# Optimization experiments

Measured on AMD Instinct MI355X. Metric: run time of the kernel, lower is better.

The kernel has to match this reference:

```python
import jax, jax.numpy as jnp
import numpy as np

B, N, D, H = 4, 2048, 512, 8
HD = D // H  # 64


def setup_inputs() -> dict:
    key = jax.random.key(0)
    ks = jax.random.split(key, 12)
    s = 0.02
    return {
        "x": jax.random.normal(ks[0], (B, N, D), jnp.float32),
        "freqs": jax.random.normal(ks[1], (B, N, HD // 2), jnp.float32),
        # weights stored as (in, out); torch Linear applies x @ W.T + b
        "wqkv_w": jax.random.normal(ks[2], (D, 3 * D), jnp.float32) * s,
        "wqkv_b": jax.random.normal(ks[3], (3 * D,), jnp.float32) * s,
        "out_w": jax.random.normal(ks[4], (D, D), jnp.float32) * s,
        "out_b": jax.random.normal(ks[5], (D,), jnp.float32) * s,
        "ffn1_w": jax.random.normal(ks[6], (2 * D, 2 * D), jnp.float32) * s,
        "ffn1_b": jax.random.normal(ks[7], (2 * D,), jnp.float32) * s,
        "ln_g": jnp.ones((2 * D,), jnp.float32),
        "ln_b": jnp.zeros((2 * D,), jnp.float32),
        "ffn2_w": jax.random.normal(ks[8], (2 * D, D), jnp.float32) * s,
        "ffn2_b": jax.random.normal(ks[9], (D,), jnp.float32) * s,
    }


def _rope(t, cos, sin):
    # t: [B,H,N,HD]; cos/sin: [B,1,N,HD/2]
    x1, x2 = t[..., ::2], t[..., 1::2]
    return jnp.stack([x1 * cos - x2 * sin, x1 * sin + x2 * cos], axis=-1).reshape(t.shape)


def reference(x, freqs, wqkv_w, wqkv_b, out_w, out_b,
              ffn1_w, ffn1_b, ln_g, ln_b, ffn2_w, ffn2_b):
    b, n, d = x.shape
    h, hd = H, d // H
    qkv = x @ wqkv_w + wqkv_b                      # [B,N,3D]
    q, k, v = jnp.split(qkv, 3, axis=-1)
    to_heads = lambda t: t.reshape(b, n, h, hd).transpose(0, 2, 1, 3)  # [B,H,N,HD]
    q, k, v = to_heads(q), to_heads(k), to_heads(v)
    cos = jnp.cos(freqs)[:, None]                  # [B,1,N,HD/2]
    sin = jnp.sin(freqs)[:, None]
    q = _rope(q, cos, sin)
    k = _rope(k, cos, sin)
    scale = hd ** -0.5
    attn = jax.nn.softmax(jnp.einsum('bhqd,bhkd->bhqk', q, k) * scale, axis=-1)
    msg = jnp.einsum('bhqk,bhkd->bhqd', attn, v).transpose(0, 2, 1, 3).reshape(b, n, d)
    msg = msg @ out_w + out_b
    # FFN on concat([x, msg]): Linear -> LayerNorm -> GELU(exact) -> Linear
    hcat = jnp.concatenate([x, msg], axis=-1) @ ffn1_w + ffn1_b   # [B,N,2D]
    mu = hcat.mean(-1, keepdims=True)
    var = hcat.var(-1, keepdims=True)
    hcat = (hcat - mu) * jax.lax.rsqrt(var + 1e-5) * ln_g + ln_b
    hcat = jax.nn.gelu(hcat, approximate=False)
    return x + hcat @ ffn2_w + ffn2_b
```

## Files before the change

### kernel.cpp

```cpp
#include <hip/hip_runtime.h>
#include <hip/hip_bf16.h>
#include <math.h>

typedef __bf16 bf16;
typedef __bf16 bf16x2 __attribute__((ext_vector_type(2)));
typedef __bf16 bf16x4 __attribute__((ext_vector_type(4)));
typedef __bf16 bf16x8 __attribute__((ext_vector_type(8)));
typedef float f32x4 __attribute__((ext_vector_type(4)));
typedef float f32x16 __attribute__((ext_vector_type(16)));

#define MFMA16(a, b, c) __builtin_amdgcn_mfma_f32_16x16x32_bf16(a, b, c, 0, 0, 0)
#define MFMA32(a, b, c) __builtin_amdgcn_mfma_f32_32x32x16_bf16(a, b, c, 0, 0, 0)


__global__ __launch_bounds__(256) void prep_kernel(
    const float* __restrict__ wqkv_w, const float* __restrict__ out_w,
    const float* __restrict__ ffn1_w, const float* __restrict__ ffn2_w,
    const float* __restrict__ x, const float* __restrict__ freqs,
    const float* __restrict__ ffn1_b, const float* __restrict__ out_b,
    bf16* __restrict__ wqkv_t, bf16* __restrict__ ffn2_t,
    bf16* __restrict__ fused_t, bf16* __restrict__ ffn1bt,
    bf16* __restrict__ out_cast, bf16* __restrict__ cat,
    float* __restrict__ bias_f, unsigned* __restrict__ tab)
{
    const int bid = blockIdx.x, tid = threadIdx.x;
    __shared__ bf16 tile[32][33];
    __shared__ float red[256];
    if (bid >= 6672) {
        int i = (bid - 6672) * 1024 + tid * 4;
        const float4 f = *(const float4*)(&freqs[i]);
        float s0, c0, s1, c1, s2, c2, s3, c3;
        __sincosf(f.x, &s0, &c0); __sincosf(f.y, &s1, &c1);
        __sincosf(f.z, &s2, &c2); __sincosf(f.w, &s3, &c3);
        union { bf16x2 h2; unsigned u; } p0, p1, p2, p3;
        p0.h2[0] = (bf16)c0; p0.h2[1] = (bf16)s0;
        p1.h2[0] = (bf16)c1; p1.h2[1] = (bf16)s1;
        p2.h2[0] = (bf16)c2; p2.h2[1] = (bf16)s2;
        p3.h2[0] = (bf16)c3; p3.h2[1] = (bf16)s3;
        uint4 o = {p0.u, p1.u, p2.u, p3.u};
        *(uint4*)(&tab[i]) = o;
        return;
    }
    if (bid >= 6656) {
        const int n = (bid - 6656) * 64 + (tid & 63);
        const int ic = tid >> 6;
        float acc = 0.f;
#pragma unroll 8
        for (int i = ic * 128; i < ic * 128 + 128; i++)
            acc += out_b[i] * ffn1_w[(size_t)(512 + i) * 1024 + n];
        red[tid] = acc;
        __syncthreads();
        if (tid < 64)
            bias_f[n] = ffn1_b[n] + red[tid] + red[tid + 64] + red[tid + 128] + red[tid + 192];
        return;
    }
    if (bid >= 2560) {
        int i = (bid - 2560) * 256 + tid;
        int row = i >> 7, col = (i & 127) << 2;
        const float4 v = *(const float4*)(&x[(size_t)row * 512 + col]);
        bf16x4 o; o[0] = (bf16)v.x; o[1] = (bf16)v.y; o[2] = (bf16)v.z; o[3] = (bf16)v.w;
        *(bf16x4*)(&cat[(size_t)row * 1024 + col]) = o;
        return;
    }
    if (bid >= 2304) {
        int i = (bid - 2304) * 1024 + tid * 4;
        const float4 v = *(const float4*)(&out_w[i]);
        bf16x4 o; o[0] = (bf16)v.x; o[1] = (bf16)v.y; o[2] = (bf16)v.z; o[3] = (bf16)v.w;
        *(bf16x4*)(&out_cast[i]) = o;
        return;
    }
    const float* src; bf16* dst; int C, ldd, bx, by;
    if (bid < 768)       { src = wqkv_w;            dst = wqkv_t;  C = 1536; ldd = 512;  int r = bid;        bx = r % 48; by = r / 48; }
    else if (bid < 1280) { src = ffn2_w;            dst = ffn2_t;  C = 512;  ldd = 1024; int r = bid - 768;  bx = r % 16; by = r / 16; }
    else if (bid < 1792) { src = ffn1_w;            dst = fused_t; C = 1024; ldd = 1024; int r = bid - 1280; bx = r % 32; by = r / 32; }
    else                 { src = ffn1_w + 512*1024; dst = ffn1bt;  C = 1024; ldd = 512;  int r = bid - 1792; bx = r % 32; by = r / 32; }
    const int tx = tid & 31, ty = tid >> 5;
    const int xx = bx * 32 + tx;
#pragma unroll
    for (int j = 0; j < 4; j++)
        tile[ty + 8 * j][tx] = (bf16)src[(size_t)(by * 32 + ty + 8 * j) * C + xx];
    __syncthreads();
    const int x2 = by * 32 + tx;
#pragma unroll
    for (int j = 0; j < 4; j++)
        dst[(size_t)(bx * 32 + ty + 8 * j) * ldd + x2] = tile[tx][ty + 8 * j];
}

__global__ __launch_bounds__(256) void qkv_wcomb_kernel(
    const bf16* __restrict__ cat, const bf16* __restrict__ wqkv_t,
    const float* __restrict__ wqkv_b, const unsigned* __restrict__ tab,
    bf16* __restrict__ qbuf, bf16* __restrict__ kbuf, bf16* __restrict__ vbuf,
    const bf16* __restrict__ ffn1bt, const bf16* __restrict__ out_cast,
    bf16* __restrict__ fused_t)
{
    const int bid = blockIdx.x;
    const bool isqkv = bid < 768;
    const bf16* A; const bf16* Bt; int lda, m0, n0;
    if (isqkv) { A = cat;    lda = 1024; Bt = wqkv_t;   n0 = (bid % 12) * 128; m0 = (bid / 12) * 128; }
    else       { int r = bid - 768;
                 A = ffn1bt; lda = 512;  Bt = out_cast; n0 = (r & 3) * 128;    m0 = (r >> 2) * 128; }
    const int K = 512;

    const int tid = threadIdx.x;
    const int lane = tid & 63, wave = tid >> 6;
    const int wm = wave >> 1, wn = wave & 1;
    const int l15 = lane & 15, quad = lane >> 4;

    __shared__ __align__(16) char smem[16384];
    bf16* As = (bf16*)smem;
    bf16* Bs = (bf16*)(smem + 8192);
    unsigned* tabs = (unsigned*)smem;

    const int c0 = tid, c1 = tid + 256;
    const int r0 = c0 >> 2, kc0 = (c0 & 3) << 3;
    const int r1 = c1 >> 2, kc1 = (c1 & 3) << 3;
    const bf16* pA0 = &A[(size_t)(m0 + r0) * lda + kc0];
    const bf16* pA1 = &A[(size_t)(m0 + r1) * lda + kc1];
    const bf16* pB0 = &Bt[(size_t)(n0 + r0) * K + kc0];
    const bf16* pB1 = &Bt[(size_t)(n0 + r1) * K + kc1];

    const f32x4 zero = {0.f, 0.f, 0.f, 0.f};
    f32x4 acc[4][4];
#pragma unroll
    for (int i = 0; i < 4; i++)
#pragma unroll
        for (int j = 0; j < 4; j++) acc[i][j] = zero;

    bf16x8 ra0 = *(const bf16x8*)pA0;
    bf16x8 ra1 = *(const bf16x8*)pA1;
    bf16x8 rb0 = *(const bf16x8*)pB0;
    bf16x8 rb1 = *(const bf16x8*)pB1;

    for (int k0 = 0; k0 < K; k0 += 32) {
        __syncthreads();
        *(bf16x8*)(&As[c0 * 8]) = ra0;
        *(bf16x8*)(&As[c1 * 8]) = ra1;
        *(bf16x8*)(&Bs[c0 * 8]) = rb0;
        *(bf16x8*)(&Bs[c1 * 8]) = rb1;
        __syncthreads();
        if (k0 + 32 < K) {
            ra0 = *(const bf16x8*)(pA0 + k0 + 32);
            ra1 = *(const bf16x8*)(pA1 + k0 + 32);
            rb0 = *(const bf16x8*)(pB0 + k0 + 32);
            rb1 = *(const bf16x8*)(pB1 + k0 + 32);
        }
        bf16x8 af[4], bfv[4];
#pragma unroll
        for (int t = 0; t < 4; t++) {
            af[t]  = *(const bf16x8*)(&As[(wm * 64 + t * 16 + l15) * 32 + quad * 8]);
            bfv[t] = *(const bf16x8*)(&Bs[(wn * 64 + t * 16 + l15) * 32 + quad * 8]);
        }
#pragma unroll
        for (int mt = 0; mt < 4; mt++)
#pragma unroll
            for (int nt = 0; nt < 4; nt++)
                acc[mt][nt] = MFMA16(af[mt], bfv[nt], acc[mt][nt]);
    }

    const int row_base = m0 + wm * 64;
    const int col_base = n0 + wn * 64;

    if (isqkv) {
        const int sector = col_base >> 9;
        const bool dorope = sector < 2;
        if (dorope) {
            __syncthreads();
#pragma unroll
            for (int ps = 0; ps < 4; ps++) {
                int idx = ps * 1024 + tid * 4;
                *(uint4*)(&tabs[idx]) = *(const uint4*)(&tab[(size_t)m0 * 32 + idx]);
            }
            __syncthreads();
        }
        const float SCQ = 0.125f * 1.44269504089f;
        bf16* dstbase = (sector == 0) ? qbuf : (sector == 1 ? kbuf : vbuf);
#pragma unroll
        for (int nt = 0; nt < 4; nt++) {
            const int col = col_base + nt * 16 + l15;
            const int cq = col & 511;
            const int h = cq >> 6, hd = cq & 63;
            const float bv = wqkv_b[col];
            const int ihalf = hd >> 1;
            const bool odd = (hd & 1) != 0;
#pragma unroll
            for (int mt = 0; mt < 4; mt++) {
#pragma unroll
                for (int r = 0; r < 4; r++) {
                    const int mrow = row_base + mt * 16 + quad * 4 + r;
                    float v = acc[mt][nt][r] + bv;
                    float o = v;
                    if (dorope) {
                        float p = __shfl_xor(v, 1);
                        const int rl = wm * 64 + mt * 16 + quad * 4 + r;
                        union { unsigned u; bf16x2 h2; } t2;
                        t2.u = tabs[rl * 32 + ihalf];
                        float cs = t2.h2[0], sn = t2.h2[1];
                        o = odd ? (p * sn + v * cs) : (v * cs - p * sn);
                        if (sector == 0) o *= SCQ;
                    }
                    const int b = mrow >> 11, n = mrow & 2047;
                    dstbase[(((size_t)b * 8 + h) * 2048 + n) * 64 + hd] = (bf16)o;
                }
            }
        }
    } else {
#pragma unroll
        for (int nt = 0; nt < 4; nt++) {
            const int col = col_base + nt * 16 + l15;
#pragma unroll
            for (int mt = 0; mt < 4; mt++) {
#pragma unroll
                for (int r = 0; r < 4; r++) {
                    const int row = row_base + mt * 16 + quad * 4 + r;
                    fused_t[(size_t)row * 1024 + 512 + col] = (bf16)acc[mt][nt][r];
                }
            }
        }
    }
}

template <int MODE>
__global__ __launch_bounds__(256) void gemm_mfma(
    const bf16* __restrict__ A, int lda, const bf16* __restrict__ Bt,
    const float* __restrict__ bias, void* __restrict__ outv,
    const float* __restrict__ auxf, int K)
{
    const int tid = threadIdx.x;
    const int lane = tid & 63, wave = tid >> 6;
    const int wm = wave >> 1, wn = wave & 1;
    const int l15 = lane & 15, quad = lane >> 4;
    const int m0 = blockIdx.y * 128;
    const int n0 = blockIdx.x * 128;

    __shared__ bf16 As[128 * 72];
    __shared__ bf16 Bs[128 * 72];

    int row[4], kc[4];
    const bf16 *pA[4], *pB[4];
#pragma unroll
    for (int i = 0; i < 4; i++) {
        int c = tid + i * 256;
        row[i] = c >> 3; kc[i] = (c & 7) << 3;
        pA[i] = &A[(size_t)(m0 + row[i]) * lda + kc[i]];
        pB[i] = &Bt[(size_t)(n0 + row[i]) * K + kc[i]];
    }

    const f32x4 zero = {0.f, 0.f, 0.f, 0.f};
    f32x4 acc[4][4];
#pragma unroll
    for (int i = 0; i < 4; i++)
#pragma unroll
        for (int j = 0; j < 4; j++) acc[i][j] = zero;

    bf16x8 ra[4], rb[4];
#pragma unroll
    for (int i = 0; i < 4; i++) { ra[i] = *(const bf16x8*)pA[i]; rb[i] = *(const bf16x8*)pB[i]; }

    for (int k0 = 0; k0 < K; k0 += 64) {
        __syncthreads();
#pragma unroll
        for (int i = 0; i < 4; i++) {
            *(bf16x8*)(&As[row[i] * 72 + kc[i]]) = ra[i];
            *(bf16x8*)(&Bs[row[i] * 72 + kc[i]]) = rb[i];
        }
        __syncthreads();
        if (k0 + 64 < K) {
#pragma unroll
            for (int i = 0; i < 4; i++) {
                ra[i] = *(const bf16x8*)(pA[i] + k0 + 64);
                rb[i] = *(const bf16x8*)(pB[i] + k0 + 64);
            }
        }
#pragma unroll
        for (int kk = 0; kk < 2; kk++) {
            bf16x8 af[4], bfv[4];
#pragma unroll
            for (int t = 0; t < 4; t++) {
                af[t]  = *(const bf16x8*)(&As[(wm * 64 + t * 16 + l15) * 72 + kk * 32 + quad * 8]);
                bfv[t] = *(const bf16x8*)(&Bs[(wn * 64 + t * 16 + l15) * 72 + kk * 32 + quad * 8]);
            }
#pragma unroll
            for (int mt = 0; mt < 4; mt++)
#pragma unroll
                for (int nt = 0; nt < 4; nt++)
                    acc[mt][nt] = MFMA16(af[mt], bfv[nt], acc[mt][nt]);
        }
    }

    const int row_base = m0 + wm * 64;
    const int col_base = n0 + wn * 64;
#pragma unroll
    for (int nt = 0; nt < 4; nt++) {
        const int col = col_base + nt * 16 + l15;
        const float bv = bias[col];
#pragma unroll
        for (int mt = 0; mt < 4; mt++) {
#pragma unroll
            for (int r = 0; r < 4; r++) {
                const int row2 = row_base + mt * 16 + quad * 4 + r;
                float v = acc[mt][nt][r] + bv;
                if constexpr (MODE == 2) {
                    ((bf16*)outv)[(size_t)row2 * 1024 + col] = (bf16)v;
                } else {
                    v += auxf[(size_t)row2 * 512 + col];
                    ((float*)outv)[(size_t)row2 * 512 + col] = v;
                }
            }
        }
    }
}

__global__ __launch_bounds__(512) void attn_kernel(const bf16* __restrict__ qb,
                                                   const bf16* __restrict__ kb,
                                                   const bf16* __restrict__ vb,
                                                   bf16* __restrict__ cat)
{
    __shared__ __align__(16) char smem[53248];
    bf16* Ks   = (bf16*)smem;
    bf16* Vts0 = (bf16*)(smem + 18432);
    bf16* Vts1 = (bf16*)(smem + 35840);

    const int tid = threadIdx.x, lane = tid & 63, wave = tid >> 6;
    const int l31 = lane & 31, half = lane >> 5;
    const int qg = wave >> 2, kh = wave & 3;
    const int bh = blockIdx.x >> 5, qt = blockIdx.x & 31;
    const int b = bh >> 3, h = bh & 7;
    const size_t base = (size_t)bh * 2048 * 64;
    const int m0 = qt * 64 + qg * 32;

    bf16x8 aq[4];
#pragma unroll
    for (int k4 = 0; k4 < 4; k4++)
        aq[k4] = *(const bf16x8*)(&qb[base + (size_t)(m0 + l31) * 64 + k4 * 16 + half * 8]);

    f32x16 accO[2];
#pragma unroll
    for (int i = 0; i < 16; i++) { accO[0][i] = 0.f; accO[1][i] = 0.f; }
    float lsum = 0.f;

    int krow[2], kcol[2];
#pragma unroll
    for (int i = 0; i < 2; i++) { int c = tid + i * 512; krow[i] = c >> 3; kcol[i] = (c & 7) << 3; }
    const int vpr = tid & 63, vdg = tid >> 6;

    bf16x8 kreg[2], vr0, vr1;
    auto prefetch = [&](int key0) {
#pragma unroll
        for (int i = 0; i < 2; i++)
            kreg[i] = *(const bf16x8*)(&kb[base + (size_t)(key0 + krow[i]) * 64 + kcol[i]]);
        vr0 = *(const bf16x8*)(&vb[base + (size_t)(key0 + 2 * vpr) * 64 + vdg * 8]);
        vr1 = *(const bf16x8*)(&vb[base + (size_t)(key0 + 2 * vpr + 1) * 64 + vdg * 8]);
    };

    const int ko = kh * 32;
    union Bu { bf16x8 v; unsigned u[4]; };
    Bu B0p, B1p;
    auto pv = [&](const bf16* Vr) {
#pragma unroll
        for (int dh = 0; dh < 2; dh++) {
            bf16x8 av0 = *(const bf16x8*)(&Vr[(dh * 32 + l31) * 136 + ko + half * 8]);
            bf16x8 av1 = *(const bf16x8*)(&Vr[(dh * 32 + l31) * 136 + ko + 16 + half * 8]);
            accO[dh] = MFMA32(av0, B0p.v, accO[dh]);
            accO[dh] = MFMA32(av1, B1p.v, accO[dh]);
        }
    };

    prefetch(0);
#pragma unroll
    for (int kt = 0; kt < 16; kt++) {
        bf16* Vw = (kt & 1) ? Vts1 : Vts0;
        bf16* Vr = (kt & 1) ? Vts0 : Vts1;
        __syncthreads();
#pragma unroll
        for (int i = 0; i < 2; i++)
            *(bf16x8*)(&Ks[krow[i] * 72 + kcol[i]]) = kreg[i];
#pragma unroll
        for (int j = 0; j < 8; j++) {
            bf16x2 pr; pr[0] = vr0[j]; pr[1] = vr1[j];
            *(bf16x2*)(&Vw[(vdg * 8 + j) * 136 + 2 * vpr]) = pr;
        }
        __syncthreads();
        if (kt < 15) prefetch((kt + 1) * 128);

        f32x16 s;
#pragma unroll
        for (int i = 0; i < 16; i++) s[i] = 0.f;
#pragma unroll
        for (int k4 = 0; k4 < 4; k4++) {
            bf16x8 ak = *(const bf16x8*)(&Ks[(ko + l31) * 72 + k4 * 16 + half * 8]);
            s = MFMA32(ak, aq[k4], s);
        }
        if (kt > 0) pv(Vr);
        float p[16];
#pragma unroll
        for (int r = 0; r < 16; r++) p[r] = __builtin_amdgcn_exp2f(s[r]);
        lsum += (((p[0] + p[1]) + (p[2] + p[3])) + ((p[4] + p[5]) + (p[6] + p[7])))
              + (((p[8] + p[9]) + (p[10] + p[11])) + ((p[12] + p[13]) + (p[14] + p[15])));
        unsigned pk[8];
#pragma unroll
        for (int i2 = 0; i2 < 8; i2++) {
            union { bf16x2 hh; unsigned u; } t;
            t.hh[0] = (bf16)p[2 * i2]; t.hh[1] = (bf16)p[2 * i2 + 1];
            pk[i2] = t.u;
        }
        const unsigned sa = half ? pk[0] : pk[2];
        const unsigned sb = half ? pk[1] : pk[3];
        const unsigned sc2 = half ? pk[4] : pk[6];
        const unsigned sd = half ? pk[5] : pk[7];
        const unsigned ra = (unsigned)__shfl_xor((int)sa, 32);
        const unsigned rb = (unsigned)__shfl_xor((int)sb, 32);
        const unsigned rc = (unsigned)__shfl_xor((int)sc2, 32);
        const unsigned rd = (unsigned)__shfl_xor((int)sd, 32);
        B0p.u[0] = half ? ra : pk[0];
        B0p.u[1] = half ? rb : pk[1];
        B0p.u[2] = half ? pk[2] : ra;
        B0p.u[3] = half ? pk[3] : rb;
        B1p.u[0] = half ? rc : pk[4];
        B1p.u[1] = half ? rd : pk[5];
        B1p.u[2] = half ? pk[6] : rc;
        B1p.u[3] = half ? pk[7] : rd;
    }
    pv(Vts1);

    auto slotp = [&](int s2) { return (float*)smem + ((s2 * 2 + qg) * 64 + lane) * 33; };
    __syncthreads();
    if (kh == 1 || kh == 3) {
        float* pr2 = slotp(kh >> 1);
#pragma unroll
        for (int dh = 0; dh < 2; dh++)
#pragma unroll
            for (int r = 0; r < 16; r++) pr2[dh * 16 + r] = accO[dh][r];
        pr2[32] = lsum;
    }
    __syncthreads();
    if (kh == 0 || kh == 2) {
        float* pr2 = slotp(kh >> 1);
#pragma unroll
        for (int dh = 0; dh < 2; dh++)
#pragma unroll
            for (int r = 0; r < 16; r++) accO[dh][r] += pr2[dh * 16 + r];
        lsum += pr2[32];
    }
    __syncthreads();
    if (kh == 2) {
        float* pr2 = slotp(0);
#pragma unroll
        for (int dh = 0; dh < 2; dh++)
#pragma unroll
            for (int r = 0; r < 16; r++) pr2[dh * 16 + r] = accO[dh][r];
        pr2[32] = lsum;
    }
    __syncthreads();
    if (kh == 0) {
        float* pr2 = slotp(0);
#pragma unroll
        for (int dh = 0; dh < 2; dh++)
#pragma unroll
            for (int r = 0; r < 16; r++) accO[dh][r] += pr2[dh * 16 + r];
        lsum += pr2[32];
        lsum += __shfl_xor(lsum, 32);
        const float inv = 1.0f / lsum;
        const int n = m0 + l31;
        bf16* aor = cat + ((size_t)b * 2048 + n) * 1024 + 512 + h * 64;
#pragma unroll
        for (int dh = 0; dh < 2; dh++) {
#pragma unroll
            for (int g = 0; g < 4; g++) {
                bf16x4 o4;
#pragma unroll
                for (int e = 0; e < 4; e++) o4[e] = (bf16)(accO[dh][g * 4 + e] * inv);
                *(bf16x4*)(&aor[dh * 32 + g * 8 + half * 4]) = o4;
            }
        }
    }
}

__global__ __launch_bounds__(256) void ln_gelu_kernel(bf16* __restrict__ hb,
                                                      const float* __restrict__ g,
                                                      const float* __restrict__ bt)
{
    const int row = blockIdx.x, tid = threadIdx.x;
    const int lane = tid & 63, wave = tid >> 6;
    bf16* hr = hb + (size_t)row * 1024;
    bf16x4 hv = *(const bf16x4*)(&hr[tid * 4]);
    float v0 = hv[0], v1 = hv[1], v2 = hv[2], v3 = hv[3];
    float s = v0 + v1 + v2 + v3;
    float q = v0 * v0 + v1 * v1 + v2 * v2 + v3 * v3;
    for (int o = 32; o; o >>= 1) { s += __shfl_xor(s, o); q += __shfl_xor(q, o); }
    __shared__ float red[8];
    if (lane == 0) { red[wave] = s; red[4 + wave] = q; }
    __syncthreads();
    s = red[0] + red[1] + red[2] + red[3];
    q = red[4] + red[5] + red[6] + red[7];
    const float mu = s * (1.f / 1024.f);
    const float rstd = rsqrtf(q * (1.f / 1024.f) - mu * mu + 1e-5f);
    const float4 gv = *(const float4*)(&g[tid * 4]);
    const float4 bv = *(const float4*)(&bt[tid * 4]);
    float vv[4] = {v0, v1, v2, v3};
    const float gg[4] = {gv.x, gv.y, gv.z, gv.w};
    const float bb[4] = {bv.x, bv.y, bv.z, bv.w};
    bf16x4 o4;
#pragma unroll
    for (int i = 0; i < 4; i++) {
        float y = (vv[i] - mu) * rstd * gg[i] + bb[i];
        float t = 1.5957691216f * y * (1.0f + 0.044715f * y * y);
        float e = __builtin_amdgcn_exp2f(-1.44269504089f * t);
        o4[i] = (bf16)(y * __builtin_amdgcn_rcpf(1.0f + e));
    }
    *(bf16x4*)(&hr[tid * 4]) = o4;
}

extern "C" void kernel_launch(void* const* d_in, const int* in_sizes, int n_in,
                              void* d_out, int out_size, void* d_ws, size_t ws_size,
                              hipStream_t stream) {
    (void)in_sizes; (void)n_in; (void)out_size; (void)ws_size;
    const float* x      = (const float*)d_in[0];
    const float* freqs  = (const float*)d_in[1];
    const float* wqkv_w = (const float*)d_in[2];
    const float* wqkv_b = (const float*)d_in[3];
    const float* out_w  = (const float*)d_in[4];
    const float* out_b  = (const float*)d_in[5];
    const float* ffn1_w = (const float*)d_in[6];
    const float* ffn1_b = (const float*)d_in[7];
    const float* ln_g   = (const float*)d_in[8];
    const float* ln_b   = (const float*)d_in[9];
    const float* ffn2_w = (const float*)d_in[10];
    const float* ffn2_b = (const float*)d_in[11];
    float* out = (float*)d_out;
    bf16* ws   = (bf16*)d_ws;

    bf16* wqkv_t   = ws;
    bf16* ffn2_t   = wqkv_t + 1536 * 512;
    bf16* fused_t  = ffn2_t + 512 * 1024;
    bf16* ffn1bt   = fused_t + 1024 * 1024;
    bf16* out_cast = ffn1bt + 1024 * 512;
    bf16* cat      = out_cast + 512 * 512;
    bf16* qbuf     = cat + (size_t)8192 * 1024;
    bf16* kbuf     = qbuf + (size_t)8192 * 512;
    bf16* vbuf     = kbuf + (size_t)8192 * 512;
    float* bias_f  = (float*)(vbuf + (size_t)8192 * 512);
    unsigned* tab  = (unsigned*)(bias_f + 1024);
    bf16* hbuf     = qbuf;

    prep_kernel<<<6928, 256, 0, stream>>>(wqkv_w, out_w, ffn1_w, ffn2_w, x, freqs,
                                          ffn1_b, out_b,
                                          wqkv_t, ffn2_t, fused_t, ffn1bt, out_cast, cat,
                                          bias_f, tab);
    qkv_wcomb_kernel<<<800, 256, 0, stream>>>(cat, wqkv_t, wqkv_b, tab, qbuf, kbuf, vbuf,
                                              ffn1bt, out_cast, fused_t);
    attn_kernel<<<1024, 512, 0, stream>>>(qbuf, kbuf, vbuf, cat);
    gemm_mfma<2><<<dim3(8, 64), 256, 0, stream>>>(cat, 1024, fused_t, bias_f, hbuf, nullptr, 1024);
    ln_gelu_kernel<<<8192, 256, 0, stream>>>(hbuf, ln_g, ln_b);
    gemm_mfma<3><<<dim3(4, 64), 256, 0, stream>>>(hbuf, 1024, ffn2_t, ffn2_b, out, x, 1024);
}
```

Before: 246.6 us.

## Load K fragments straight to registers and stage V in per-wave LDS

The attention kernel no longer stages a shared K tile and a double-buffered V tile for the whole block. Each wave now loads its own K MFMA fragments directly from global memory into registers, and transposes its own V slice into a private LDS region. This removes both __syncthreads per key tile and shrinks LDS use. The cost is redundant global/L2 traffic, since waves that share a key slice now each fetch it, and K fragment loads are strided by row rather than fully coalesced.

```diff
diff --git a/kernel.cpp b/kernel.cpp
--- a/kernel.cpp
+++ b/kernel.cpp
@@ -315,10 +315,7 @@
                                                    const bf16* __restrict__ vb,
                                                    bf16* __restrict__ cat)
 {
-    __shared__ __align__(16) char smem[53248];
-    bf16* Ks   = (bf16*)smem;
-    bf16* Vts0 = (bf16*)(smem + 18432);
-    bf16* Vts1 = (bf16*)(smem + 35840);
+    __shared__ __align__(16) char smem[38912];
 
     const int tid = threadIdx.x, lane = tid & 63, wave = tid >> 6;
     const int l31 = lane & 31, half = lane >> 5;
@@ -327,6 +324,9 @@
     const int b = bh >> 3, h = bh & 7;
     const size_t base = (size_t)bh * 2048 * 64;
     const int m0 = qt * 64 + qg * 32;
+    const int ko = kh * 32;
+
+    bf16* Vq = (bf16*)(smem + wave * 4864);
 
     bf16x8 aq[4];
 #pragma unroll
@@ -338,59 +338,57 @@
     for (int i = 0; i < 16; i++) { accO[0][i] = 0.f; accO[1][i] = 0.f; }
     float lsum = 0.f;
 
-    int krow[2], kcol[2];
-#pragma unroll
-    for (int i = 0; i < 2; i++) { int c = tid + i * 512; krow[i] = c >> 3; kcol[i] = (c & 7) << 3; }
-    const int vpr = tid & 63, vdg = tid >> 6;
-
-    bf16x8 kreg[2], vr0, vr1;
-    auto prefetch = [&](int key0) {
-#pragma unroll
-        for (int i = 0; i < 2; i++)
-            kreg[i] = *(const bf16x8*)(&kb[base + (size_t)(key0 + krow[i]) * 64 + kcol[i]]);
-        vr0 = *(const bf16x8*)(&vb[base + (size_t)(key0 + 2 * vpr) * 64 + vdg * 8]);
-        vr1 = *(const bf16x8*)(&vb[base + (size_t)(key0 + 2 * vpr + 1) * 64 + vdg * 8]);
+    const bf16* kf0 = kb + base + (size_t)(ko + l31) * 64 + half * 8;
+    const int p2 = lane & 15, dg = lane >> 4;
+    const bf16* vf0 = vb + base + (size_t)(ko + 2 * p2) * 64 + dg * 16;
+
+    bf16x8 kfrag[4], v00, v01, v10, v11;
+    auto loadK = [&](int key0) {
+#pragma unroll
+        for (int k4 = 0; k4 < 4; k4++)
+            kfrag[k4] = *(const bf16x8*)(kf0 + (size_t)key0 * 64 + k4 * 16);
     };
-
-    const int ko = kh * 32;
+    auto loadV = [&](int key0) {
+        const bf16* p = vf0 + (size_t)key0 * 64;
+        v00 = *(const bf16x8*)(p);
+        v01 = *(const bf16x8*)(p + 8);
+        v10 = *(const bf16x8*)(p + 64);
+        v11 = *(const bf16x8*)(p + 72);
+    };
+
     union Bu { bf16x8 v; unsigned u[4]; };
     Bu B0p, B1p;
-    auto pv = [&](const bf16* Vr) {
+    auto pv = [&]() {
 #pragma unroll
         for (int dh = 0; dh < 2; dh++) {
-            bf16x8 av0 = *(const bf16x8*)(&Vr[(dh * 32 + l31) * 136 + ko + half * 8]);
-            bf16x8 av1 = *(const bf16x8*)(&Vr[(dh * 32 + l31) * 136 + ko + 16 + half * 8]);
+            bf16x8 av0 = *(const bf16x8*)(&Vq[(dh * 32 + l31) * 38 + half * 8]);
+            bf16x8 av1 = *(const bf16x8*)(&Vq[(dh * 32 + l31) * 38 + 16 + half * 8]);
             accO[dh] = MFMA32(av0, B0p.v, accO[dh]);
             accO[dh] = MFMA32(av1, B1p.v, accO[dh]);
         }
     };
 
-    prefetch(0);
+    loadK(0); loadV(0);
 #pragma unroll
     for (int kt = 0; kt < 16; kt++) {
-        bf16* Vw = (kt & 1) ? Vts1 : Vts0;
-        bf16* Vr = (kt & 1) ? Vts0 : Vts1;
-        __syncthreads();
-#pragma unroll
-        for (int i = 0; i < 2; i++)
-            *(bf16x8*)(&Ks[krow[i] * 72 + kcol[i]]) = kreg[i];
+        f32x16 s;
+#pragma unroll
+        for (int i = 0; i < 16; i++) s[i] = 0.f;
+#pragma unroll
+        for (int k4 = 0; k4 < 4; k4++) s = MFMA32(kfrag[k4], aq[k4], s);
+        if (kt < 15) loadK((kt + 1) * 128);
+        if (kt > 0) pv();
 #pragma unroll
         for (int j = 0; j < 8; j++) {
-            bf16x2 pr; pr[0] = vr0[j]; pr[1] = vr1[j];
-            *(bf16x2*)(&Vw[(vdg * 8 + j) * 136 + 2 * vpr]) = pr;
-        }
-        __syncthreads();
-        if (kt < 15) prefetch((kt + 1) * 128);
-
-        f32x16 s;
-#pragma unroll
-        for (int i = 0; i < 16; i++) s[i] = 0.f;
-#pragma unroll
-        for (int k4 = 0; k4 < 4; k4++) {
-            bf16x8 ak = *(const bf16x8*)(&Ks[(ko + l31) * 72 + k4 * 16 + half * 8]);
-            s = MFMA32(ak, aq[k4], s);
-        }
-        if (kt > 0) pv(Vr);
+            bf16x2 pr; pr[0] = v00[j]; pr[1] = v10[j];
+            *(bf16x2*)(&Vq[(dg * 16 + j) * 38 + 2 * p2]) = pr;
+        }
+#pragma unroll
+        for (int j = 0; j < 8; j++) {
+            bf16x2 pr; pr[0] = v01[j]; pr[1] = v11[j];
+            *(bf16x2*)(&Vq[(dg * 16 + 8 + j) * 38 + 2 * p2]) = pr;
+        }
+        if (kt < 15) loadV((kt + 1) * 128);
         float p[16];
 #pragma unroll
         for (int r = 0; r < 16; r++) p[r] = __builtin_amdgcn_exp2f(s[r]);
@@ -420,7 +418,7 @@
         B1p.u[2] = half ? pk[6] : rc;
         B1p.u[3] = half ? pk[7] : rd;
     }
-    pv(Vts1);
+    pv();
 
     auto slotp = [&](int s2) { return (float*)smem + ((s2 * 2 + qg) * 64 + lane) * 33; };
     __syncthreads();
```

New measurement: 313.9 us. +27.3%, slower.
